# Kernel optimization log

Measured on AMD Instinct MI355X. Metric: run time of the kernel, lower is better.

Reference implementation:

```python
import jax, jax.numpy as jnp
import numpy as np

GROUP = 32  # quantization group size along K, fixed by the call site


def setup_inputs() -> dict:
    key = jax.random.key(0)
    k1, k2, k3 = jax.random.split(key, 3)
    M, K, N = 1, 8192, 16384
    A = jax.random.normal(k1, (M, K), dtype=jnp.float16)
    # packed int4 weights: each byte holds two nibbles -> [N, K//2]
    B = jax.random.randint(k2, (N, K // 2), 0, 256, dtype=jnp.int32)
    scalesAndZeros = (jax.random.normal(k3, (N, K // GROUP, 2), dtype=jnp.float16))
    return {"A": A, "B": B, "scalesAndZeros": scalesAndZeros}


def _dequant(B, scalesAndZeros):
    # B: [N, K//2] bytes, two int4 values per byte (low nibble = even k)
    N, Kh = B.shape
    K = Kh * 2
    low = B & 0xF
    high = (B >> 4) & 0xF
    q = jnp.stack([low, high], axis=-1).reshape(N, K).astype(jnp.float32) - 8.0
    scales = scalesAndZeros[..., 0].astype(jnp.float32)  # [N, K//GROUP]
    zeros = scalesAndZeros[..., 1].astype(jnp.float32)   # [N, K//GROUP]
    qg = q.reshape(N, K // GROUP, GROUP)
    W = qg * scales[:, :, None] + zeros[:, :, None]       # [N, K//GROUP, GROUP]
    return W.reshape(N, K)


def reference(A, B, scalesAndZeros):
    # int4 weight-only quantized GEMV: out[m, n] = sum_k A[m, k] * dequant(W)[n, k]
    W = _dequant(B, scalesAndZeros)                        # [N, K] fp32
    out = jnp.einsum("mk,nk->mn", A.astype(jnp.float32), W)
    return out.astype(A.dtype)                             # [1, N] fp16
```

## Files before the change

kernel.cpp:

```cpp
#include <hip/hip_runtime.h>


#define ROWS   2
#define TPB    256
#define PASSES 4

typedef int   ivec4 __attribute__((ext_vector_type(4)));
typedef float fvec2 __attribute__((ext_vector_type(2)));

__global__ __launch_bounds__(TPB, 8) void gemv_w4hi(
    const float4* __restrict__ A4,
    const ivec4*  __restrict__ B,
    const fvec2*  __restrict__ SZ,
    float* __restrict__ out,
    int N)
{
    const int t  = threadIdx.x;
    const int n0 = blockIdx.x * ROWS;

    const ivec4* B0 = B + (size_t)n0 * 1024 + t;
    ivec4 b[PASSES][ROWS];
#pragma unroll
    for (int p = 0; p < PASSES; ++p)
#pragma unroll
        for (int r = 0; r < ROWS; ++r)
            b[p][r] = __builtin_nontemporal_load(&B0[(size_t)r * 1024 + p * 256]);

    float acc[ROWS];
#pragma unroll
    for (int r = 0; r < ROWS; ++r) acc[r] = 0.0f;

#pragma unroll
    for (int p = 0; p < PASSES; ++p) {
        const int i = t + 256 * p;
        const float4 x = A4[2 * i];
        const float4 y = A4[2 * i + 1];
        const float a0 = x.x, a1 = x.y, a2 = x.z, a3 = x.w;
        const float a4 = y.x, a5 = y.y, a6 = y.z, a7 = y.w;
        const float sA = ((a0 + a1) + (a2 + a3)) + ((a4 + a5) + (a6 + a7));
        const int g = i >> 2;
#pragma unroll
        for (int r = 0; r < ROWS; ++r) {
            const fvec2 sz =
                __builtin_nontemporal_load(&SZ[(size_t)(n0 + r) * 256 + g]);
            const int b0 = b[p][r][0], b1 = b[p][r][1];
            const int b2 = b[p][r][2], b3 = b[p][r][3];
            float dot = 0.0f;
            dot = fmaf(a0, (float)(b0 & 0xF),        dot);
            dot = fmaf(a1, (float)((b0 >> 4) & 0xF), dot);
            dot = fmaf(a2, (float)(b1 & 0xF),        dot);
            dot = fmaf(a3, (float)((b1 >> 4) & 0xF), dot);
            dot = fmaf(a4, (float)(b2 & 0xF),        dot);
            dot = fmaf(a5, (float)((b2 >> 4) & 0xF), dot);
            dot = fmaf(a6, (float)(b3 & 0xF),        dot);
            dot = fmaf(a7, (float)((b3 >> 4) & 0xF), dot);
            const float s  = sz[0];
            const float zz = fmaf(-8.0f, s, sz[1]);
            acc[r] = fmaf(s,  dot, acc[r]);
            acc[r] = fmaf(zz, sA,  acc[r]);
        }
    }

    __shared__ float red[ROWS][TPB / 64];
    const int lane = t & 63;
    const int w    = t >> 6;
#pragma unroll
    for (int r = 0; r < ROWS; ++r) {
        float v = acc[r];
#pragma unroll
        for (int off = 32; off > 0; off >>= 1)
            v += __shfl_down(v, off, 64);
        if (lane == 0) red[r][w] = v;
    }
    __syncthreads();
    if (t < ROWS) {
        const int n = n0 + t;
        if (n < N) {
            float v = 0.0f;
#pragma unroll
            for (int w2 = 0; w2 < TPB / 64; ++w2) v += red[t][w2];
            out[n] = v;
        }
    }
}

extern "C" void kernel_launch(void* const* d_in, const int* in_sizes, int n_in,
                              void* d_out, int out_size, void* d_ws, size_t ws_size,
                              hipStream_t stream) {
    const float4* A4 = (const float4*)d_in[0];
    const ivec4*  B  = (const ivec4*)d_in[1];
    const fvec2*  SZ = (const fvec2*)d_in[2];
    float* out = (float*)d_out;

    const int N = out_size;
    gemv_w4hi<<<N / ROWS, TPB, 0, stream>>>(A4, B, SZ, out, N);
}
```

Measured before the change: 382.5 us.

## Stream weight rows through LDS with multi-buffered async global_load_lds pipeline

```diff
diff --git a/kernel.cpp b/kernel.cpp
--- a/kernel.cpp
+++ b/kernel.cpp
@@ -1,84 +1,122 @@
 #include <hip/hip_runtime.h>
 
 
-#define ROWS   2
-#define TPB    256
-#define PASSES 4
+#define TPB   512
+#define TILES 32
+#define NBUF  4
 
 typedef int   ivec4 __attribute__((ext_vector_type(4)));
 typedef float fvec2 __attribute__((ext_vector_type(2)));
 
-__global__ __launch_bounds__(TPB, 8) void gemv_w4hi(
+__global__ __launch_bounds__(TPB, 4) void gemv_w4lds(
     const float4* __restrict__ A4,
-    const ivec4*  __restrict__ B,
-    const fvec2*  __restrict__ SZ,
+    const int*    __restrict__ B,
+    const float*  __restrict__ SZ,
     float* __restrict__ out,
     int N)
 {
-    const int t  = threadIdx.x;
-    const int n0 = blockIdx.x * ROWS;
+    const int t    = threadIdx.x;
+    const int w    = t >> 6;
+    const int lane = t & 63;
+    const int row0 = blockIdx.x * TILES;
+    const int g0   = t >> 2;
 
-    const ivec4* B0 = B + (size_t)n0 * 1024 + t;
-    ivec4 b[PASSES][ROWS];
+    __shared__ ivec4 bbuf[NBUF][1024];
+    __shared__ fvec2 szbuf[NBUF][256];
+    __shared__ float red2[TILES][8];
+
+    float a[2][8];
+    float sA[2];
 #pragma unroll
-    for (int p = 0; p < PASSES; ++p)
-#pragma unroll
-        for (int r = 0; r < ROWS; ++r)
-            b[p][r] = __builtin_nontemporal_load(&B0[(size_t)r * 1024 + p * 256]);
+    for (int j = 0; j < 2; ++j) {
+        const int i = t + 512 * j;
+        const float4 x = A4[2 * i];
+        const float4 y = A4[2 * i + 1];
+        a[j][0] = x.x; a[j][1] = x.y; a[j][2] = x.z; a[j][3] = x.w;
+        a[j][4] = y.x; a[j][5] = y.y; a[j][6] = y.z; a[j][7] = y.w;
+        sA[j] = ((x.x + x.y) + (x.z + x.w)) + ((y.x + y.y) + (y.z + y.w));
+    }
 
-    float acc[ROWS];
-#pragma unroll
-    for (int r = 0; r < ROWS; ++r) acc[r] = 0.0f;
+    auto stage = [&](int T) {
+        const int p = T & (NBUF - 1);
+        const char* gb = (const char*)B + (size_t)(row0 + T) * 16384;
+        __builtin_amdgcn_global_load_lds(
+            (const unsigned int*)(gb + w * 1024 + lane * 16),
+            (unsigned int*)&bbuf[p][w * 64], 16, 0, 0);
+        __builtin_amdgcn_global_load_lds(
+            (const unsigned int*)(gb + (w + 8) * 1024 + lane * 16),
+            (unsigned int*)&bbuf[p][(w + 8) * 64], 16, 0, 0);
+        const char* gs = (const char*)SZ + (size_t)(row0 + T) * 2048;
+        __builtin_amdgcn_global_load_lds(
+            (const unsigned int*)(gs + w * 256 + lane * 4),
+            (unsigned int*)&szbuf[p][0] + w * 64, 4, 0, 0);
+    };
+
+    stage(0); stage(1); stage(2);
 
 #pragma unroll
-    for (int p = 0; p < PASSES; ++p) {
-        const int i = t + 256 * p;
-        const float4 x = A4[2 * i];
-        const float4 y = A4[2 * i + 1];
-        const float a0 = x.x, a1 = x.y, a2 = x.z, a3 = x.w;
-        const float a4 = y.x, a5 = y.y, a6 = y.z, a7 = y.w;
-        const float sA = ((a0 + a1) + (a2 + a3)) + ((a4 + a5) + (a6 + a7));
-        const int g = i >> 2;
-#pragma unroll
-        for (int r = 0; r < ROWS; ++r) {
-            const fvec2 sz =
-                __builtin_nontemporal_load(&SZ[(size_t)(n0 + r) * 256 + g]);
-            const int b0 = b[p][r][0], b1 = b[p][r][1];
-            const int b2 = b[p][r][2], b3 = b[p][r][3];
+    for (int T = 0; T < TILES; ++T) {
+        if (T < TILES - 2)       asm volatile("s_waitcnt vmcnt(6)" ::: "memory");
+        else if (T == TILES - 2) asm volatile("s_waitcnt vmcnt(3)" ::: "memory");
+        else                     asm volatile("s_waitcnt vmcnt(0)" ::: "memory");
+        __builtin_amdgcn_s_barrier();
+        __builtin_amdgcn_sched_barrier(0);
+
+        const int p = T & (NBUF - 1);
+        const ivec4 b0 = bbuf[p][t];
+        const ivec4 b1 = bbuf[p][512 + t];
+        const fvec2 s0 = szbuf[p][g0];
+        const fvec2 s1 = szbuf[p][128 + g0];
+
+        float v = 0.0f;
+        {
+            const int c0 = b0[0], c1 = b0[1], c2 = b0[2], c3 = b0[3];
             float dot = 0.0f;
-            dot = fmaf(a0, (float)(b0 & 0xF),        dot);
-            dot = fmaf(a1, (float)((b0 >> 4) & 0xF), dot);
-            dot = fmaf(a2, (float)(b1 & 0xF),        dot);
-            dot = fmaf(a3, (float)((b1 >> 4) & 0xF), dot);
-            dot = fmaf(a4, (float)(b2 & 0xF),        dot);
-            dot = fmaf(a5, (float)((b2 >> 4) & 0xF), dot);
-            dot = fmaf(a6, (float)(b3 & 0xF),        dot);
-            dot = fmaf(a7, (float)((b3 >> 4) & 0xF), dot);
-            const float s  = sz[0];
-            const float zz = fmaf(-8.0f, s, sz[1]);
-            acc[r] = fmaf(s,  dot, acc[r]);
-            acc[r] = fmaf(zz, sA,  acc[r]);
+            dot = fmaf(a[0][0], (float)(c0 & 0xF),        dot);
+            dot = fmaf(a[0][1], (float)((c0 >> 4) & 0xF), dot);
+            dot = fmaf(a[0][2], (float)(c1 & 0xF),        dot);
+            dot = fmaf(a[0][3], (float)((c1 >> 4) & 0xF), dot);
+            dot = fmaf(a[0][4], (float)(c2 & 0xF),        dot);
+            dot = fmaf(a[0][5], (float)((c2 >> 4) & 0xF), dot);
+            dot = fmaf(a[0][6], (float)(c3 & 0xF),        dot);
+            dot = fmaf(a[0][7], (float)((c3 >> 4) & 0xF), dot);
+            v = fmaf(s0[0], dot, v);
+            v = fmaf(fmaf(-8.0f, s0[0], s0[1]), sA[0], v);
         }
-    }
+        {
+            const int c0 = b1[0], c1 = b1[1], c2 = b1[2], c3 = b1[3];
+            float dot = 0.0f;
+            dot = fmaf(a[1][0], (float)(c0 & 0xF),        dot);
+            dot = fmaf(a[1][1], (float)((c0 >> 4) & 0xF), dot);
+            dot = fmaf(a[1][2], (float)(c1 & 0xF),        dot);
+            dot = fmaf(a[1][3], (float)((c1 >> 4) & 0xF), dot);
+            dot = fmaf(a[1][4], (float)(c2 & 0xF),        dot);
+            dot = fmaf(a[1][5], (float)((c2 >> 4) & 0xF), dot);
+            dot = fmaf(a[1][6], (float)(c3 & 0xF),        dot);
+            dot = fmaf(a[1][7], (float)((c3 >> 4) & 0xF), dot);
+            v = fmaf(s1[0], dot, v);
+            v = fmaf(fmaf(-8.0f, s1[0], s1[1]), sA[1], v);
+        }
 
-    __shared__ float red[ROWS][TPB / 64];
-    const int lane = t & 63;
-    const int w    = t >> 6;
-#pragma unroll
-    for (int r = 0; r < ROWS; ++r) {
-        float v = acc[r];
 #pragma unroll
         for (int off = 32; off > 0; off >>= 1)
             v += __shfl_down(v, off, 64);
-        if (lane == 0) red[r][w] = v;
+        if (lane == 0) red2[T][w] = v;
+
+        asm volatile("s_waitcnt lgkmcnt(0)" ::: "memory");
+        __builtin_amdgcn_sched_barrier(0);
+        __builtin_amdgcn_s_barrier();
+
+        if (T + 3 < TILES) stage(T + 3);
     }
+
     __syncthreads();
-    if (t < ROWS) {
-        const int n = n0 + t;
+    if (t < TILES) {
+        const int n = row0 + t;
         if (n < N) {
             float v = 0.0f;
 #pragma unroll
-            for (int w2 = 0; w2 < TPB / 64; ++w2) v += red[t][w2];
+            for (int w2 = 0; w2 < 8; ++w2) v += red2[t][w2];
             out[n] = v;
         }
     }
@@ -88,10 +126,10 @@
                               void* d_out, int out_size, void* d_ws, size_t ws_size,
                               hipStream_t stream) {
     const float4* A4 = (const float4*)d_in[0];
-    const ivec4*  B  = (const ivec4*)d_in[1];
-    const fvec2*  SZ = (const fvec2*)d_in[2];
+    const int*    B  = (const int*)d_in[1];
+    const float*  SZ = (const float*)d_in[2];
     float* out = (float*)d_out;
 
     const int N = out_size;
-    gemv_w4hi<<<N / ROWS, TPB, 0, stream>>>(A4, B, SZ, out, N);
+    gemv_w4lds<<<N / TILES, TPB, 0, stream>>>(A4, B, SZ, out, N);
 }
```

Result: no change. 382.7 us (+0.1%).
